# Optimization experiments

Hardware: AMD Instinct MI355X
Metric: run time of the kernel (lower is better)

Reference implementation:

```python
import jax, jax.numpy as jnp
import numpy as np

CHUNK = 64  # output-column tile to bound the [M, K, CHUNK] intermediate


def _mam(A, B):
    """Multiply-and-max/min 'matmul': C[m,n] = max_k(A[m,k]*B[k,n]) + min_k(A[m,k]*B[k,n]).
    A: [M, K], B: [K, N]. Tiled over N to avoid materializing [M, K, N]."""
    M, K = A.shape
    N = B.shape[1]
    assert N % CHUNK == 0
    # [N/CHUNK, K, CHUNK]
    B_tiles = B.reshape(K, N // CHUNK, CHUNK).transpose(1, 0, 2)

    def step(carry, B_blk):
        # prod: [M, K, CHUNK]
        prod = A[:, :, None] * B_blk[None, :, :]
        out = prod.max(axis=1) + prod.min(axis=1)  # [M, CHUNK]
        return carry, out

    _, tiles = jax.lax.scan(step, 0, B_tiles)  # [N/CHUNK, M, CHUNK]
    return tiles.transpose(1, 0, 2).reshape(M, N)


def setup_inputs() -> dict:
    key = jax.random.key(0)
    k1, k2, k3 = jax.random.split(key, 3)
    M, K, N = 2048, 1024, 1024
    x = jax.random.normal(k1, (M, K), dtype=jnp.float32)
    # torch stores weight as [out_features, in_features]
    weight = jax.random.normal(k2, (N, K), dtype=jnp.float32) * (1.0 / np.sqrt(K))
    bias = jax.random.normal(k3, (N,), dtype=jnp.float32) * (1.0 / np.sqrt(K))
    return {"x": x, "weight": weight, "bias": bias}


def reference(x, weight, bias):
    # beta == 0 (beta=False): forward is MAM(x, W^T) + bias
    C = _mam(x, weight.T)
    return C + bias[None, :]
```

## Files before the change

### kernel.cpp

```cpp
#include <hip/hip_runtime.h>
#include <math.h>


#define BM 32
#define BN 64
#define BK 32
#define LDSA 36
#define LDSW 68

__device__ __forceinline__ void mam_update(float& mx, float& mn, float p0, float p1) {
    float nmx, nmn;
    asm("v_max3_f32 %0, %1, %2, %3" : "=v"(nmx) : "v"(p0), "v"(p1), "v"(mx));
    asm("v_min3_f32 %0, %1, %2, %3" : "=v"(nmn) : "v"(p0), "v"(p1), "v"(mn));
    mx = nmx;
    mn = nmn;
}

__global__ __launch_bounds__(256) void mam_kernel(
    const float* __restrict__ A,
    const float* __restrict__ W,
    const float* __restrict__ bias,
    float* __restrict__ C,
    int M, int N, int K)
{
    __shared__ float As[BK][LDSA];
    __shared__ float Ws[BK][LDSW];

    const int t  = threadIdx.x;
    const int tx = t & 15;
    const int ty = t >> 4;
    const int m0 = blockIdx.y * BM;
    const int n0 = blockIdx.x * BN;

    const int r  = t >> 3;
    const int kq = t & 7;

    const float* Aptr = A + (size_t)(m0 + r) * K + kq * 4;
    const float* Wptr = W + (size_t)(n0 + r) * K + kq * 4;

    float vmax[2][4], vmin[2][4];
#pragma unroll
    for (int i = 0; i < 2; ++i)
#pragma unroll
        for (int j = 0; j < 4; ++j) {
            vmax[i][j] = -INFINITY;
            vmin[i][j] =  INFINITY;
        }

    for (int k0 = 0; k0 < K; k0 += BK) {
        float4 a0 = *(const float4*)(Aptr);
        float4 w0 = *(const float4*)(Wptr);
        float4 w1 = *(const float4*)(Wptr + (size_t)32 * K);
        Aptr += BK;
        Wptr += BK;

        const int kk = kq * 4;
        As[kk + 0][r] = a0.x;
        As[kk + 1][r] = a0.y;
        As[kk + 2][r] = a0.z;
        As[kk + 3][r] = a0.w;

        Ws[kk + 0][r]      = w0.x;
        Ws[kk + 1][r]      = w0.y;
        Ws[kk + 2][r]      = w0.z;
        Ws[kk + 3][r]      = w0.w;
        Ws[kk + 0][r + 32] = w1.x;
        Ws[kk + 1][r + 32] = w1.y;
        Ws[kk + 2][r + 32] = w1.z;
        Ws[kk + 3][r + 32] = w1.w;

        __syncthreads();

#pragma unroll
        for (int k = 0; k < BK; k += 2) {
            float2 ta0 = *(const float2*)&As[k    ][ty * 2];
            float2 ta1 = *(const float2*)&As[k + 1][ty * 2];
            float4 tb0 = *(const float4*)&Ws[k    ][tx * 4];
            float4 tb1 = *(const float4*)&Ws[k + 1][tx * 4];

            float a0v[2] = {ta0.x, ta0.y};
            float a1v[2] = {ta1.x, ta1.y};
            float b0v[4] = {tb0.x, tb0.y, tb0.z, tb0.w};
            float b1v[4] = {tb1.x, tb1.y, tb1.z, tb1.w};

#pragma unroll
            for (int i = 0; i < 2; ++i) {
#pragma unroll
                for (int j = 0; j < 4; ++j) {
                    float p0 = a0v[i] * b0v[j];
                    float p1 = a1v[i] * b1v[j];
                    mam_update(vmax[i][j], vmin[i][j], p0, p1);
                }
            }
        }

        __syncthreads();
    }

    float4 bv = *(const float4*)(bias + n0 + tx * 4);
#pragma unroll
    for (int i = 0; i < 2; ++i) {
        float4 o;
        o.x = vmax[i][0] + vmin[i][0] + bv.x;
        o.y = vmax[i][1] + vmin[i][1] + bv.y;
        o.z = vmax[i][2] + vmin[i][2] + bv.z;
        o.w = vmax[i][3] + vmin[i][3] + bv.w;
        *(float4*)(C + (size_t)(m0 + ty * 2 + i) * N + n0 + tx * 4) = o;
    }
}

extern "C" void kernel_launch(void* const* d_in, const int* in_sizes, int n_in,
                              void* d_out, int out_size, void* d_ws, size_t ws_size,
                              hipStream_t stream) {
    const float* x    = (const float*)d_in[0];
    const float* w    = (const float*)d_in[1];
    const float* bias = (const float*)d_in[2];
    float* out = (float*)d_out;

    const int N = in_sizes[2];
    const int K = in_sizes[1] / N;
    const int M = in_sizes[0] / K;

    dim3 grid(N / BN, M / BM);
    dim3 block(256);
    mam_kernel<<<grid, block, 0, stream>>>(x, w, bias, out, M, N, K);
}
```

Baseline: 180.2 us.

## Use 64x64 tiles with intra-block split-K across wavefronts and 8x8 microtiles

Replaces the 32x64 tile kernel with a 64x64 tile kernel in which each of the four wavefronts processes a quarter of K using its own LDS buffers. The wavefronts need no block barriers in the main loop, and each thread holds an 8x8 max/min register tile. Partial max/min results are combined through LDS at the end before adding bias. This aims to raise arithmetic intensity per LDS load and remove per-iteration block syncs. In exchange it uses much more register and LDS space, which may limit occupancy. A fallback kernel with 64x64 tiles handles shapes that do not fit.

Result: faster. 154.8 us (-14.1%).

```diff
diff --git a/kernel.cpp b/kernel.cpp
--- a/kernel.cpp
+++ b/kernel.cpp
@@ -2,13 +2,11 @@
 #include <math.h>
 
 
-#define BM 32
-#define BN 64
-#define BK 32
-#define LDSA 36
-#define LDSW 68
-
-__device__ __forceinline__ void mam_update(float& mx, float& mn, float p0, float p1) {
+#define TS 64
+#define BK 16
+#define LDSP 68
+
+__device__ __forceinline__ void mam_upd(float& mx, float& mn, float p0, float p1) {
     float nmx, nmn;
     asm("v_max3_f32 %0, %1, %2, %3" : "=v"(nmx) : "v"(p0), "v"(p1), "v"(mx));
     asm("v_min3_f32 %0, %1, %2, %3" : "=v"(nmn) : "v"(p0), "v"(p1), "v"(mn));
@@ -16,96 +14,237 @@
     mn = nmn;
 }
 
-__global__ __launch_bounds__(256) void mam_kernel(
-    const float* __restrict__ A,
-    const float* __restrict__ W,
-    const float* __restrict__ bias,
-    float* __restrict__ C,
+__global__ __launch_bounds__(256, 2) void mam_sk(
+    const float* __restrict__ A, const float* __restrict__ W,
+    const float* __restrict__ bias, float* __restrict__ C,
     int M, int N, int K)
 {
-    __shared__ float As[BK][LDSA];
-    __shared__ float Ws[BK][LDSW];
+    __shared__ float sA[4][BK][LDSP];
+    __shared__ float sW[4][BK][LDSP];
+    __shared__ float cmx[TS * TS];
+    __shared__ float cmn[TS * TS];
+
+    const int t    = threadIdx.x;
+    const int w    = t >> 6;
+    const int lane = t & 63;
+    const int ty   = lane >> 3;
+    const int tx   = lane & 7;
+    const int m0   = blockIdx.y * TS;
+    const int n0   = blockIdx.x * TS;
+    const int kc   = K >> 2;
+    const int kb0  = w * kc;
+
+    const int sr = lane >> 2;
+    const int sc = lane & 3;
+
+    const float* Ap = A + (size_t)(m0 + sr) * K + kb0 + sc * 4;
+    const float* Wp = W + (size_t)(n0 + sr) * K + kb0 + sc * 4;
+
+    float mx[8][8], mn[8][8];
+#pragma unroll
+    for (int i = 0; i < 8; ++i)
+#pragma unroll
+        for (int j = 0; j < 8; ++j) {
+            mx[i][j] = -INFINITY;
+            mn[i][j] =  INFINITY;
+        }
+
+    float4 ra[4], rw[4];
+#pragma unroll
+    for (int q = 0; q < 4; ++q) {
+        ra[q] = *(const float4*)(Ap + (size_t)q * 16 * K);
+        rw[q] = *(const float4*)(Wp + (size_t)q * 16 * K);
+    }
+    Ap += BK;
+    Wp += BK;
+
+    const int nStages = kc / BK;
+    for (int s = 0; s < nStages; ++s) {
+#pragma unroll
+        for (int q = 0; q < 4; ++q) {
+            const int mI = sr + q * 16;
+            sA[w][sc * 4 + 0][mI] = ra[q].x;
+            sA[w][sc * 4 + 1][mI] = ra[q].y;
+            sA[w][sc * 4 + 2][mI] = ra[q].z;
+            sA[w][sc * 4 + 3][mI] = ra[q].w;
+            sW[w][sc * 4 + 0][mI] = rw[q].x;
+            sW[w][sc * 4 + 1][mI] = rw[q].y;
+            sW[w][sc * 4 + 2][mI] = rw[q].z;
+            sW[w][sc * 4 + 3][mI] = rw[q].w;
+        }
+        if (s + 1 < nStages) {
+#pragma unroll
+            for (int q = 0; q < 4; ++q) {
+                ra[q] = *(const float4*)(Ap + (size_t)q * 16 * K);
+                rw[q] = *(const float4*)(Wp + (size_t)q * 16 * K);
+            }
+            Ap += BK;
+            Wp += BK;
+        }
+
+#pragma unroll
+        for (int k = 0; k < BK; k += 2) {
+            float4 a00 = *(const float4*)&sA[w][k    ][ty * 8];
+            float4 a01 = *(const float4*)&sA[w][k    ][ty * 8 + 4];
+            float4 a10 = *(const float4*)&sA[w][k + 1][ty * 8];
+            float4 a11 = *(const float4*)&sA[w][k + 1][ty * 8 + 4];
+            float4 w00 = *(const float4*)&sW[w][k    ][tx * 8];
+            float4 w01 = *(const float4*)&sW[w][k    ][tx * 8 + 4];
+            float4 w10 = *(const float4*)&sW[w][k + 1][tx * 8];
+            float4 w11 = *(const float4*)&sW[w][k + 1][tx * 8 + 4];
+
+            float a0[8] = {a00.x, a00.y, a00.z, a00.w, a01.x, a01.y, a01.z, a01.w};
+            float a1[8] = {a10.x, a10.y, a10.z, a10.w, a11.x, a11.y, a11.z, a11.w};
+            float b0[8] = {w00.x, w00.y, w00.z, w00.w, w01.x, w01.y, w01.z, w01.w};
+            float b1[8] = {w10.x, w10.y, w10.z, w10.w, w11.x, w11.y, w11.z, w11.w};
+
+#pragma unroll
+            for (int i = 0; i < 8; ++i)
+#pragma unroll
+                for (int j = 0; j < 8; ++j) {
+                    float p0 = a0[i] * b0[j];
+                    float p1 = a1[i] * b1[j];
+                    mam_upd(mx[i][j], mn[i][j], p0, p1);
+                }
+        }
+    }
+
+    for (int rnd = 0; rnd < 4; ++rnd) {
+        if (w == rnd) {
+#pragma unroll
+            for (int i = 0; i < 8; ++i)
+#pragma unroll
+                for (int j = 0; j < 8; ++j) {
+                    const int idx = (ty * 8 + i) * TS + tx * 8 + j;
+                    if (rnd == 0) {
+                        cmx[idx] = mx[i][j];
+                        cmn[idx] = mn[i][j];
+                    } else {
+                        cmx[idx] = fmaxf(cmx[idx], mx[i][j]);
+                        cmn[idx] = fminf(cmn[idx], mn[i][j]);
+                    }
+                }
+        }
+        __syncthreads();
+    }
+
+    float4 blo = *(const float4*)(bias + n0 + tx * 8);
+    float4 bhi = *(const float4*)(bias + n0 + tx * 8 + 4);
+#pragma unroll
+    for (int i2 = 0; i2 < 2; ++i2) {
+        const int i   = w * 2 + i2;
+        const int row = ty * 8 + i;
+        const int idx = row * TS + tx * 8;
+        float4 o0, o1;
+        o0.x = cmx[idx + 0] + cmn[idx + 0] + blo.x;
+        o0.y = cmx[idx + 1] + cmn[idx + 1] + blo.y;
+        o0.z = cmx[idx + 2] + cmn[idx + 2] + blo.z;
+        o0.w = cmx[idx + 3] + cmn[idx + 3] + blo.w;
+        o1.x = cmx[idx + 4] + cmn[idx + 4] + bhi.x;
+        o1.y = cmx[idx + 5] + cmn[idx + 5] + bhi.y;
+        o1.z = cmx[idx + 6] + cmn[idx + 6] + bhi.z;
+        o1.w = cmx[idx + 7] + cmn[idx + 7] + bhi.w;
+        float4* p = (float4*)(C + (size_t)(m0 + row) * N + n0 + tx * 8);
+        p[0] = o0;
+        p[1] = o1;
+    }
+}
+
+#define BM 64
+#define BN 64
+#define FBK 32
+#define LDSW 68
+
+__global__ __launch_bounds__(256) void mam_fallback(
+    const float* __restrict__ A, const float* __restrict__ W,
+    const float* __restrict__ bias, float* __restrict__ C,
+    int M, int N, int K)
+{
+    __shared__ float Asf[FBK][LDSW];
+    __shared__ float Wsf[FBK][LDSW];
 
     const int t  = threadIdx.x;
     const int tx = t & 15;
     const int ty = t >> 4;
     const int m0 = blockIdx.y * BM;
     const int n0 = blockIdx.x * BN;
-
     const int r  = t >> 3;
     const int kq = t & 7;
 
     const float* Aptr = A + (size_t)(m0 + r) * K + kq * 4;
     const float* Wptr = W + (size_t)(n0 + r) * K + kq * 4;
 
-    float vmax[2][4], vmin[2][4];
-#pragma unroll
-    for (int i = 0; i < 2; ++i)
+    float vmax[4][4], vmin[4][4];
+#pragma unroll
+    for (int i = 0; i < 4; ++i)
 #pragma unroll
         for (int j = 0; j < 4; ++j) {
             vmax[i][j] = -INFINITY;
             vmin[i][j] =  INFINITY;
         }
 
-    for (int k0 = 0; k0 < K; k0 += BK) {
+    for (int k0 = 0; k0 < K; k0 += FBK) {
         float4 a0 = *(const float4*)(Aptr);
+        float4 a1 = *(const float4*)(Aptr + (size_t)32 * K);
         float4 w0 = *(const float4*)(Wptr);
         float4 w1 = *(const float4*)(Wptr + (size_t)32 * K);
-        Aptr += BK;
-        Wptr += BK;
+        Aptr += FBK;
+        Wptr += FBK;
 
         const int kk = kq * 4;
-        As[kk + 0][r] = a0.x;
-        As[kk + 1][r] = a0.y;
-        As[kk + 2][r] = a0.z;
-        As[kk + 3][r] = a0.w;
-
-        Ws[kk + 0][r]      = w0.x;
-        Ws[kk + 1][r]      = w0.y;
-        Ws[kk + 2][r]      = w0.z;
-        Ws[kk + 3][r]      = w0.w;
-        Ws[kk + 0][r + 32] = w1.x;
-        Ws[kk + 1][r + 32] = w1.y;
-        Ws[kk + 2][r + 32] = w1.z;
-        Ws[kk + 3][r + 32] = w1.w;
+        Asf[kk + 0][r]      = a0.x;
+        Asf[kk + 1][r]      = a0.y;
+        Asf[kk + 2][r]      = a0.z;
+        Asf[kk + 3][r]      = a0.w;
+        Asf[kk + 0][r + 32] = a1.x;
+        Asf[kk + 1][r + 32] = a1.y;
+        Asf[kk + 2][r + 32] = a1.z;
+        Asf[kk + 3][r + 32] = a1.w;
+
+        Wsf[kk + 0][r]      = w0.x;
+        Wsf[kk + 1][r]      = w0.y;
+        Wsf[kk + 2][r]      = w0.z;
+        Wsf[kk + 3][r]      = w0.w;
+        Wsf[kk + 0][r + 32] = w1.x;
+        Wsf[kk + 1][r + 32] = w1.y;
+        Wsf[kk + 2][r + 32] = w1.z;
+        Wsf[kk + 3][r + 32] = w1.w;
 
         __syncthreads();
 
 #pragma unroll
-        for (int k = 0; k < BK; k += 2) {
-            float2 ta0 = *(const float2*)&As[k    ][ty * 2];
-            float2 ta1 = *(const float2*)&As[k + 1][ty * 2];
-            float4 tb0 = *(const float4*)&Ws[k    ][tx * 4];
-            float4 tb1 = *(const float4*)&Ws[k + 1][tx * 4];
-
-            float a0v[2] = {ta0.x, ta0.y};
-            float a1v[2] = {ta1.x, ta1.y};
+        for (int k = 0; k < FBK; k += 2) {
+            float4 ta0 = *(const float4*)&Asf[k    ][ty * 4];
+            float4 ta1 = *(const float4*)&Asf[k + 1][ty * 4];
+            float4 tb0 = *(const float4*)&Wsf[k    ][tx * 4];
+            float4 tb1 = *(const float4*)&Wsf[k + 1][tx * 4];
+
+            float a0v[4] = {ta0.x, ta0.y, ta0.z, ta0.w};
+            float a1v[4] = {ta1.x, ta1.y, ta1.z, ta1.w};
             float b0v[4] = {tb0.x, tb0.y, tb0.z, tb0.w};
             float b1v[4] = {tb1.x, tb1.y, tb1.z, tb1.w};
 
 #pragma unroll
-            for (int i = 0; i < 2; ++i) {
+            for (int i = 0; i < 4; ++i)
 #pragma unroll
                 for (int j = 0; j < 4; ++j) {
                     float p0 = a0v[i] * b0v[j];
                     float p1 = a1v[i] * b1v[j];
-                    mam_update(vmax[i][j], vmin[i][j], p0, p1);
+                    mam_upd(vmax[i][j], vmin[i][j], p0, p1);
                 }
-            }
-        }
-
+        }
         __syncthreads();
     }
 
     float4 bv = *(const float4*)(bias + n0 + tx * 4);
 #pragma unroll
-    for (int i = 0; i < 2; ++i) {
+    for (int i = 0; i < 4; ++i) {
         float4 o;
         o.x = vmax[i][0] + vmin[i][0] + bv.x;
         o.y = vmax[i][1] + vmin[i][1] + bv.y;
         o.z = vmax[i][2] + vmin[i][2] + bv.z;
         o.w = vmax[i][3] + vmin[i][3] + bv.w;
-        *(float4*)(C + (size_t)(m0 + ty * 2 + i) * N + n0 + tx * 4) = o;
+        *(float4*)(C + (size_t)(m0 + ty * 4 + i) * N + n0 + tx * 4) = o;
     }
 }
 
@@ -121,7 +260,13 @@
     const int K = in_sizes[1] / N;
     const int M = in_sizes[0] / K;
 
-    dim3 grid(N / BN, M / BM);
-    dim3 block(256);
-    mam_kernel<<<grid, block, 0, stream>>>(x, w, bias, out, M, N, K);
-}
+    const bool fast_ok = (K % (4 * BK) == 0) && (M % TS == 0) && (N % TS == 0);
+
+    if (fast_ok) {
+        dim3 grid(N / TS, M / TS);
+        mam_sk<<<grid, 256, 0, stream>>>(x, w, bias, out, M, N, K);
+    } else {
+        dim3 grid(N / BN, M / BM);
+        mam_fallback<<<grid, 256, 0, stream>>>(x, w, bias, out, M, N, K);
+    }
+}
```
